# Kernel optimization log

Measured on AMD Instinct MI355X. Metric: run time of the kernel, lower is better.

Reference implementation:

```python
import jax, jax.numpy as jnp
import numpy as np

NUM_CLASSES = 19
EPS = 1e-8  # torch cosine_similarity eps


def setup_inputs() -> dict:
    key = jax.random.key(0)
    k1, k2 = jax.random.split(key)
    inputs = jax.random.normal(k1, (8, 256, 128, 128), dtype=jnp.float32)  # (B, D, H, W)
    targets = jax.random.randint(k2, (8, 128, 128), 0, NUM_CLASSES)        # (B, H, W)
    return {"inputs": inputs, "targets": targets}


def reference(inputs, targets):
    B, D, H, W = inputs.shape
    C = NUM_CLASSES
    # (N, D) pixel embeddings and (N,) labels
    feats = jnp.transpose(inputs, (0, 2, 3, 1)).reshape(-1, D)
    labels = targets.reshape(-1)

    # per-class centroids: sum of embeddings / max(count, 1)  (matches sum_pixel = max(mask.sum(), 1))
    counts = jax.ops.segment_sum(jnp.ones(labels.shape, jnp.float32), labels, num_segments=C)  # (C,)
    sums = jax.ops.segment_sum(feats, labels, num_segments=C)                                   # (C, D)
    centers = sums / jnp.maximum(counts, 1.0)[:, None]
    present = counts > 0  # classes absent from the batch are skipped in both loss terms

    # ---- sim_loss: sum over present classes of mean_{pixels of class i} (1 - cos(center_i, feat)) ----
    cen_px = centers[labels]                                   # (N, D)
    dot = jnp.sum(feats * cen_px, axis=1)
    n_f = jnp.sqrt(jnp.sum(feats * feats, axis=1))
    n_c = jnp.sqrt(jnp.sum(cen_px * cen_px, axis=1))
    cos_px = dot / jnp.maximum(n_f * n_c, EPS)
    per_class = jax.ops.segment_sum(1.0 - cos_px, labels, num_segments=C) / jnp.maximum(counts, 1.0)
    sim_loss = jnp.sum(jnp.where(present, per_class, 0.0))

    # ---- diff_loss: for each present i, mean_j over all C classes of
    #      (1 - cos(center_j, center_i)) if j == i else relu(cos(center_j, center_i)) ----
    n_cen = jnp.sqrt(jnp.sum(centers * centers, axis=1))       # (C,)
    S = (centers @ centers.T) / jnp.maximum(n_cen[:, None] * n_cen[None, :], EPS)  # (C, C)
    eye = jnp.eye(C, dtype=bool)
    per_pair = jnp.where(eye, 1.0 - S, jnp.maximum(S, 0.0))    # row i = losses vs class i
    per_i = jnp.mean(per_pair, axis=1)                          # mean reduction over C rows
    diff_loss = jnp.sum(jnp.where(present, per_i, 0.0))

    return jnp.reshape(diff_loss + sim_loss, (1,))  # torch returns a shape-(1,) tensor
```

## Files before the change

kernel.cpp:

```cpp
#include <hip/hip_runtime.h>
#include <math.h>

#define D_DIM 256
#define HW 16384
#define C 19
#define EPS 1e-8f

#define S_SC 1048576.0f
#define IS_S (1.0f/1048576.0f)
#define U_SC 16777216.0f
#define IS_U (1.0f/16777216.0f)

#define OFF_S      0
#define OFF_U      4864
#define OFF_CNT    9728
#define OFF_IO     9760
#define OFF_PNF    140832
#define PNF_STRIDE 8256
#define OFF_PS     4367904
#define OFF_PU     4445728

__global__ __launch_bounds__(256) void kA_stream(const float* __restrict__ in,
                                                 const int* __restrict__ tgt,
                                                 int* __restrict__ wsi) {
    __shared__ int sS[8 * 161];
    const int tid = threadIdx.x;
    const int bid = blockIdx.x;
    const int b = bid >> 6, s = (bid >> 1) & 31, h = bid & 1;
    const int copy = tid & 7;
    for (int i = tid; i < 8 * 161; i += 256) sS[i] = 0;
    __syncthreads();

    const int hwb = (h << 13) + (tid << 2);
    const int pb  = (b << 14) + hwb;
    int4 lab[8];
    #pragma unroll
    for (int it = 0; it < 8; ++it) lab[it] = *(const int4*)(tgt + pb + (it << 10));

    const float* base = in + (((size_t)((b << 8) + (s << 3))) << 14) + hwb;
    float4 nf[8];
    #pragma unroll
    for (int it = 0; it < 8; ++it) nf[it] = make_float4(0.f, 0.f, 0.f, 0.f);

    #pragma unroll
    for (int d = 0; d < 8; ++d) {
        float4 v[8];
        #pragma unroll
        for (int it = 0; it < 8; ++it)
            v[it] = *(const float4*)(base + ((size_t)d << 14) + (it << 10));
        const int sb = copy * 161 + d * 20;
        #pragma unroll
        for (int it = 0; it < 8; ++it) {
            nf[it].x += v[it].x * v[it].x; nf[it].y += v[it].y * v[it].y;
            nf[it].z += v[it].z * v[it].z; nf[it].w += v[it].w * v[it].w;
            atomicAdd(&sS[sb + lab[it].x], __float2int_rn(v[it].x * S_SC));
            atomicAdd(&sS[sb + lab[it].y], __float2int_rn(v[it].y * S_SC));
            atomicAdd(&sS[sb + lab[it].z], __float2int_rn(v[it].z * S_SC));
            atomicAdd(&sS[sb + lab[it].w], __float2int_rn(v[it].w * S_SC));
        }
    }

    float* pnf = (float*)wsi + OFF_PNF
               + (size_t)(((b << 1) + h) * 32 + s) * PNF_STRIDE;
    #pragma unroll
    for (int it = 0; it < 8; ++it)
        *(float4*)(pnf + (it << 10) + (tid << 2)) = nf[it];

    __syncthreads();
    if (tid < 152) {
        const int d = tid / 19, l = tid - d * 19;
        int acc = 0;
        #pragma unroll
        for (int c = 0; c < 8; ++c) acc += sS[c * 161 + d * 20 + l];
        wsi[OFF_PS + bid * 152 + tid] = acc;
    }
}

__global__ __launch_bounds__(256) void kA2_io(int* __restrict__ wsi) {
    float* wsf = (float*)wsi;
    const int j = blockIdx.x, tid = threadIdx.x;
    const int b = j >> 4, h = (j >> 3) & 1, ch = j & 7;
    const float* pn = wsf + OFF_PNF + (size_t)((b << 1) + h) * 32 * PNF_STRIDE
                    + (ch << 10) + (tid << 2);
    float4 acc = {0.f, 0.f, 0.f, 0.f};
    #pragma unroll 8
    for (int s = 0; s < 32; ++s) {
        float4 v = *(const float4*)(pn + (size_t)s * PNF_STRIDE);
        acc.x += v.x; acc.y += v.y; acc.z += v.z; acc.w += v.w;
    }
    float4 io;
    io.x = acc.x > 0.f ? U_SC * rsqrtf(acc.x) : 0.f;
    io.y = acc.y > 0.f ? U_SC * rsqrtf(acc.y) : 0.f;
    io.z = acc.z > 0.f ? U_SC * rsqrtf(acc.z) : 0.f;
    io.w = acc.w > 0.f ? U_SC * rsqrtf(acc.w) : 0.f;
    *(float4*)(wsf + OFF_IO + (b << 14) + (h << 13) + (ch << 10) + (tid << 2)) = io;
    if (j == 0 && tid < 32) wsi[OFF_CNT + tid] = 0;
}

__global__ __launch_bounds__(256) void kB_stream(const float* __restrict__ in,
                                                 const int* __restrict__ tgt,
                                                 int* __restrict__ wsi) {
    __shared__ int sU[8 * 161];
    __shared__ int sH[8 * 21];
    const int tid = threadIdx.x;
    const int bid = blockIdx.x;
    const int b = bid >> 6, s = (bid >> 1) & 31, h = bid & 1;
    const int copy = tid & 7;
    for (int i = tid; i < 8 * 161; i += 256) sU[i] = 0;
    if (tid < 8 * 21) sH[tid] = 0;
    __syncthreads();

    const int hwb = (h << 13) + (tid << 2);
    const int pb  = (b << 14) + hwb;
    const float* iof = (const float*)wsi + OFF_IO;
    int4   lab[8];
    float4 io4[8];
    #pragma unroll
    for (int it = 0; it < 8; ++it) {
        lab[it] = *(const int4*)(tgt + pb + (it << 10));
        io4[it] = *(const float4*)(iof + pb + (it << 10));
    }
    if (s == 0) {
        #pragma unroll
        for (int it = 0; it < 8; ++it) {
            atomicAdd(&sH[copy * 21 + lab[it].x], 1);
            atomicAdd(&sH[copy * 21 + lab[it].y], 1);
            atomicAdd(&sH[copy * 21 + lab[it].z], 1);
            atomicAdd(&sH[copy * 21 + lab[it].w], 1);
        }
    }

    const float* base = in + (((size_t)((b << 8) + (s << 3))) << 14) + hwb;
    #pragma unroll
    for (int d = 0; d < 8; ++d) {
        float4 v[8];
        #pragma unroll
        for (int it = 0; it < 8; ++it)
            v[it] = *(const float4*)(base + ((size_t)d << 14) + (it << 10));
        const int sb = copy * 161 + d * 20;
        #pragma unroll
        for (int it = 0; it < 8; ++it) {
            atomicAdd(&sU[sb + lab[it].x], __float2int_rn(v[it].x * io4[it].x));
            atomicAdd(&sU[sb + lab[it].y], __float2int_rn(v[it].y * io4[it].y));
            atomicAdd(&sU[sb + lab[it].z], __float2int_rn(v[it].z * io4[it].z));
            atomicAdd(&sU[sb + lab[it].w], __float2int_rn(v[it].w * io4[it].w));
        }
    }
    __syncthreads();
    if (tid < 152) {
        const int d = tid / 19, l = tid - d * 19;
        int acc = 0;
        #pragma unroll
        for (int c = 0; c < 8; ++c) acc += sU[c * 161 + d * 20 + l];
        wsi[OFF_PU + bid * 152 + tid] = acc;
    }
    if (s == 0 && tid < C) {
        int t = 0;
        #pragma unroll
        for (int c = 0; c < 8; ++c) t += sH[c * 21 + tid];
        atomicAdd(&wsi[OFF_CNT + tid], t);
    }
}

__global__ __launch_bounds__(256) void k1b_merge(int* __restrict__ wsi) {
    const int a = blockIdx.x >> 5, s = blockIdx.x & 31;
    const int tid = threadIdx.x;
    if (tid >= 152) return;
    const int* src = wsi + (a ? OFF_PU : OFF_PS);
    int acc = 0;
    #pragma unroll
    for (int r = 0; r < 16; ++r) {
        const int row = ((r >> 1) << 6) + (s << 1) + (r & 1);
        acc += src[row * 152 + tid];
    }
    const int d = tid / 19, l = tid - (tid / 19) * 19;
    wsi[(a ? OFF_U : OFF_S) + l * D_DIM + (s << 3) + d] = acc;
}

__global__ __launch_bounds__(512) void k2_final(const int* __restrict__ wsi,
                                                float* __restrict__ out) {
    __shared__ __align__(16) float s_cen[C * 260];
    __shared__ __align__(16) float s_u[C * 260];
    __shared__ float s_nc[C];
    __shared__ float s_cntf[C];
    __shared__ float s_pair[C * C];
    __shared__ float s_sim[C];
    const int tid = threadIdx.x;

    if (tid < C) s_cntf[tid] = (float)wsi[OFF_CNT + tid];
    __syncthreads();
    for (int i = tid; i < C * 256; i += 512) {
        int c = i >> 8, d = i & 255;
        float icnt = 1.f / fmaxf(s_cntf[c], 1.f);
        s_cen[c * 260 + d] = (float)wsi[OFF_S + i] * IS_S * icnt;
        s_u[c * 260 + d]   = (float)wsi[OFF_U + i] * IS_U;
    }
    __syncthreads();
    if (tid < C) {
        float nsq = 0.f;
        for (int d = 0; d < D_DIM; ++d) {
            float x = s_cen[tid * 260 + d];
            nsq += x * x;
        }
        s_nc[tid] = sqrtf(nsq);
    }
    __syncthreads();
    if (tid < C * C) {
        int i = tid / C, j = tid % C;
        const float4* ci = (const float4*)&s_cen[i * 260];
        const float4* cj = (const float4*)&s_cen[j * 260];
        float dot = 0.f;
        #pragma unroll 8
        for (int k = 0; k < 64; ++k) {
            float4 a = ci[k], bb = cj[k];
            dot += a.x * bb.x + a.y * bb.y + a.z * bb.z + a.w * bb.w;
        }
        float S = dot / fmaxf(s_nc[i] * s_nc[j], EPS);
        s_pair[tid] = (i == j) ? (1.f - S) : fmaxf(S, 0.f);
    } else if (tid >= 384 && tid < 384 + C) {
        int i = tid - 384;
        const float4* ci = (const float4*)&s_cen[i * 260];
        const float4* ui = (const float4*)&s_u[i * 260];
        float dot = 0.f;
        #pragma unroll 8
        for (int k = 0; k < 64; ++k) {
            float4 a = ci[k], bb = ui[k];
            dot += a.x * bb.x + a.y * bb.y + a.z * bb.z + a.w * bb.w;
        }
        s_sim[i] = (s_cntf[i] > 0.f)
                 ? (1.f - dot / fmaxf(s_nc[i] * s_cntf[i], EPS)) : 0.f;
    }
    __syncthreads();
    if (tid < C) {
        float row = 0.f;
        for (int j = 0; j < C; ++j) row += s_pair[tid * C + j];
        s_pair[tid * C] = (s_cntf[tid] > 0.f) ? (row * (1.f / (float)C)) : 0.f;
    }
    __syncthreads();
    if (tid == 0) {
        float tot = 0.f;
        for (int i = 0; i < C; ++i) tot += s_pair[i * C] + s_sim[i];
        out[0] = tot;
    }
}

extern "C" void kernel_launch(void* const* d_in, const int* in_sizes, int n_in,
                              void* d_out, int out_size, void* d_ws, size_t ws_size,
                              hipStream_t stream) {
    const float* in  = (const float*)d_in[0];
    const int*   tgt = (const int*)d_in[1];
    float* out = (float*)d_out;
    int*   wsi = (int*)d_ws;

    kA_stream<<<512, 256, 0, stream>>>(in, tgt, wsi);
    kA2_io<<<128, 256, 0, stream>>>(wsi);
    kB_stream<<<512, 256, 0, stream>>>(in, tgt, wsi);
    k1b_merge<<<64, 256, 0, stream>>>(wsi);
    k2_final<<<1, 512, 0, stream>>>(wsi, out);
}
```

Before: 229.6 us.

## Split streaming kernels into 2048 smaller blocks and move class counting to pass A

Both streaming passes now use 2048 blocks, each covering an eighth of an image's pixels for 8 channels, where before 512 blocks covered half an image. Each thread handles 2 float4 pixel groups instead of 8, which cuts register pressure and spreads work across more CUs. The class histogram moves into pass A and is written as per-block partial counts that the final kernel sums, replacing global atomics and the zeroing step. The cost is four times more partial-sum rows for the merge kernel to reduce, and more per-block setup and shared-memory reduction overhead.

```diff
diff --git a/kernel.cpp b/kernel.cpp
--- a/kernel.cpp
+++ b/kernel.cpp
@@ -13,44 +13,47 @@
 
 #define OFF_S      0
 #define OFF_U      4864
-#define OFF_CNT    9728
-#define OFF_IO     9760
-#define OFF_PNF    140832
-#define PNF_STRIDE 8256
-#define OFF_PS     4367904
-#define OFF_PU     4445728
+#define OFF_PCNT   9728
+#define OFF_IO     10944
+#define OFF_PNF    142016
+#define PNF_STRIDE 2080
+#define OFF_PS     4401856
+#define OFF_PU     4713152
+
 
 __global__ __launch_bounds__(256) void kA_stream(const float* __restrict__ in,
                                                  const int* __restrict__ tgt,
                                                  int* __restrict__ wsi) {
     __shared__ int sS[8 * 161];
+    __shared__ int sH[8 * 21];
     const int tid = threadIdx.x;
     const int bid = blockIdx.x;
-    const int b = bid >> 6, s = (bid >> 1) & 31, h = bid & 1;
+    const int b = bid >> 8, slab = (bid >> 3) & 31, oct = bid & 7;
     const int copy = tid & 7;
     for (int i = tid; i < 8 * 161; i += 256) sS[i] = 0;
-    __syncthreads();
-
-    const int hwb = (h << 13) + (tid << 2);
+    if (tid < 8 * 21) sH[tid] = 0;
+    __syncthreads();
+
+    const int hwb = (oct << 11) + (tid << 2);
     const int pb  = (b << 14) + hwb;
-    int4 lab[8];
-    #pragma unroll
-    for (int it = 0; it < 8; ++it) lab[it] = *(const int4*)(tgt + pb + (it << 10));
-
-    const float* base = in + (((size_t)((b << 8) + (s << 3))) << 14) + hwb;
-    float4 nf[8];
-    #pragma unroll
-    for (int it = 0; it < 8; ++it) nf[it] = make_float4(0.f, 0.f, 0.f, 0.f);
+    int4 lab[2];
+    #pragma unroll
+    for (int it = 0; it < 2; ++it) lab[it] = *(const int4*)(tgt + pb + (it << 10));
+
+    const float* base = in + (((size_t)((b << 8) + (slab << 3))) << 14) + hwb;
+    float4 nf[2];
+    nf[0] = make_float4(0.f, 0.f, 0.f, 0.f);
+    nf[1] = make_float4(0.f, 0.f, 0.f, 0.f);
 
     #pragma unroll
     for (int d = 0; d < 8; ++d) {
-        float4 v[8];
-        #pragma unroll
-        for (int it = 0; it < 8; ++it)
+        float4 v[2];
+        #pragma unroll
+        for (int it = 0; it < 2; ++it)
             v[it] = *(const float4*)(base + ((size_t)d << 14) + (it << 10));
         const int sb = copy * 161 + d * 20;
         #pragma unroll
-        for (int it = 0; it < 8; ++it) {
+        for (int it = 0; it < 2; ++it) {
             nf[it].x += v[it].x * v[it].x; nf[it].y += v[it].y * v[it].y;
             nf[it].z += v[it].z * v[it].z; nf[it].w += v[it].w * v[it].w;
             atomicAdd(&sS[sb + lab[it].x], __float2int_rn(v[it].x * S_SC));
@@ -60,86 +63,92 @@
         }
     }
 
-    float* pnf = (float*)wsi + OFF_PNF
-               + (size_t)(((b << 1) + h) * 32 + s) * PNF_STRIDE;
-    #pragma unroll
-    for (int it = 0; it < 8; ++it)
-        *(float4*)(pnf + (it << 10) + (tid << 2)) = nf[it];
-
+    {
+        float* pnf = (float*)wsi + OFF_PNF
+                   + (size_t)(((b << 3) + oct) * 32 + slab) * PNF_STRIDE;
+        *(float4*)(pnf + (tid << 2))        = nf[0];
+        *(float4*)(pnf + 1024 + (tid << 2)) = nf[1];
+    }
+
+    if (slab == 0) {
+        #pragma unroll
+        for (int it = 0; it < 2; ++it) {
+            atomicAdd(&sH[copy * 21 + lab[it].x], 1);
+            atomicAdd(&sH[copy * 21 + lab[it].y], 1);
+            atomicAdd(&sH[copy * 21 + lab[it].z], 1);
+            atomicAdd(&sH[copy * 21 + lab[it].w], 1);
+        }
+    }
     __syncthreads();
     if (tid < 152) {
-        const int d = tid / 19, l = tid - d * 19;
+        const int d = tid / 19, l = tid - (tid / 19) * 19;
         int acc = 0;
         #pragma unroll
         for (int c = 0; c < 8; ++c) acc += sS[c * 161 + d * 20 + l];
         wsi[OFF_PS + bid * 152 + tid] = acc;
     }
+    if (slab == 0 && tid < C) {
+        int t = 0;
+        #pragma unroll
+        for (int c = 0; c < 8; ++c) t += sH[c * 21 + tid];
+        wsi[OFF_PCNT + ((b << 3) + oct) * 19 + tid] = t;
+    }
 }
 
 __global__ __launch_bounds__(256) void kA2_io(int* __restrict__ wsi) {
     float* wsf = (float*)wsi;
-    const int j = blockIdx.x, tid = threadIdx.x;
-    const int b = j >> 4, h = (j >> 3) & 1, ch = j & 7;
-    const float* pn = wsf + OFF_PNF + (size_t)((b << 1) + h) * 32 * PNF_STRIDE
-                    + (ch << 10) + (tid << 2);
-    float4 acc = {0.f, 0.f, 0.f, 0.f};
-    #pragma unroll 8
-    for (int s = 0; s < 32; ++s) {
-        float4 v = *(const float4*)(pn + (size_t)s * PNF_STRIDE);
-        acc.x += v.x; acc.y += v.y; acc.z += v.z; acc.w += v.w;
-    }
-    float4 io;
-    io.x = acc.x > 0.f ? U_SC * rsqrtf(acc.x) : 0.f;
-    io.y = acc.y > 0.f ? U_SC * rsqrtf(acc.y) : 0.f;
-    io.z = acc.z > 0.f ? U_SC * rsqrtf(acc.z) : 0.f;
-    io.w = acc.w > 0.f ? U_SC * rsqrtf(acc.w) : 0.f;
-    *(float4*)(wsf + OFF_IO + (b << 14) + (h << 13) + (ch << 10) + (tid << 2)) = io;
-    if (j == 0 && tid < 32) wsi[OFF_CNT + tid] = 0;
+    const int boct = blockIdx.x, tid = threadIdx.x;
+    const float* pn0 = wsf + OFF_PNF + (size_t)(boct * 32) * PNF_STRIDE;
+    #pragma unroll
+    for (int it = 0; it < 2; ++it) {
+        const int j = (it << 10) + (tid << 2);
+        float4 acc = {0.f, 0.f, 0.f, 0.f};
+        #pragma unroll 8
+        for (int s = 0; s < 32; ++s) {
+            float4 v = *(const float4*)(pn0 + (size_t)s * PNF_STRIDE + j);
+            acc.x += v.x; acc.y += v.y; acc.z += v.z; acc.w += v.w;
+        }
+        float4 io;
+        io.x = acc.x > 0.f ? U_SC * rsqrtf(acc.x) : 0.f;
+        io.y = acc.y > 0.f ? U_SC * rsqrtf(acc.y) : 0.f;
+        io.z = acc.z > 0.f ? U_SC * rsqrtf(acc.z) : 0.f;
+        io.w = acc.w > 0.f ? U_SC * rsqrtf(acc.w) : 0.f;
+        *(float4*)(wsf + OFF_IO + ((boct >> 3) << 14) + ((boct & 7) << 11) + j) = io;
+    }
 }
 
 __global__ __launch_bounds__(256) void kB_stream(const float* __restrict__ in,
                                                  const int* __restrict__ tgt,
                                                  int* __restrict__ wsi) {
     __shared__ int sU[8 * 161];
-    __shared__ int sH[8 * 21];
     const int tid = threadIdx.x;
     const int bid = blockIdx.x;
-    const int b = bid >> 6, s = (bid >> 1) & 31, h = bid & 1;
+    const int b = bid >> 8, slab = (bid >> 3) & 31, oct = bid & 7;
     const int copy = tid & 7;
     for (int i = tid; i < 8 * 161; i += 256) sU[i] = 0;
-    if (tid < 8 * 21) sH[tid] = 0;
-    __syncthreads();
-
-    const int hwb = (h << 13) + (tid << 2);
+    __syncthreads();
+
+    const int hwb = (oct << 11) + (tid << 2);
     const int pb  = (b << 14) + hwb;
     const float* iof = (const float*)wsi + OFF_IO;
-    int4   lab[8];
-    float4 io4[8];
-    #pragma unroll
-    for (int it = 0; it < 8; ++it) {
+    int4   lab[2];
+    float4 io4[2];
+    #pragma unroll
+    for (int it = 0; it < 2; ++it) {
         lab[it] = *(const int4*)(tgt + pb + (it << 10));
         io4[it] = *(const float4*)(iof + pb + (it << 10));
     }
-    if (s == 0) {
-        #pragma unroll
-        for (int it = 0; it < 8; ++it) {
-            atomicAdd(&sH[copy * 21 + lab[it].x], 1);
-            atomicAdd(&sH[copy * 21 + lab[it].y], 1);
-            atomicAdd(&sH[copy * 21 + lab[it].z], 1);
-            atomicAdd(&sH[copy * 21 + lab[it].w], 1);
-        }
-    }
-
-    const float* base = in + (((size_t)((b << 8) + (s << 3))) << 14) + hwb;
+
+    const float* base = in + (((size_t)((b << 8) + (slab << 3))) << 14) + hwb;
     #pragma unroll
     for (int d = 0; d < 8; ++d) {
-        float4 v[8];
-        #pragma unroll
-        for (int it = 0; it < 8; ++it)
+        float4 v[2];
+        #pragma unroll
+        for (int it = 0; it < 2; ++it)
             v[it] = *(const float4*)(base + ((size_t)d << 14) + (it << 10));
         const int sb = copy * 161 + d * 20;
         #pragma unroll
-        for (int it = 0; it < 8; ++it) {
+        for (int it = 0; it < 2; ++it) {
             atomicAdd(&sU[sb + lab[it].x], __float2int_rn(v[it].x * io4[it].x));
             atomicAdd(&sU[sb + lab[it].y], __float2int_rn(v[it].y * io4[it].y));
             atomicAdd(&sU[sb + lab[it].z], __float2int_rn(v[it].z * io4[it].z));
@@ -148,33 +157,27 @@
     }
     __syncthreads();
     if (tid < 152) {
-        const int d = tid / 19, l = tid - d * 19;
+        const int d = tid / 19, l = tid - (tid / 19) * 19;
         int acc = 0;
         #pragma unroll
         for (int c = 0; c < 8; ++c) acc += sU[c * 161 + d * 20 + l];
         wsi[OFF_PU + bid * 152 + tid] = acc;
     }
-    if (s == 0 && tid < C) {
-        int t = 0;
-        #pragma unroll
-        for (int c = 0; c < 8; ++c) t += sH[c * 21 + tid];
-        atomicAdd(&wsi[OFF_CNT + tid], t);
-    }
-}
-
-__global__ __launch_bounds__(256) void k1b_merge(int* __restrict__ wsi) {
-    const int a = blockIdx.x >> 5, s = blockIdx.x & 31;
+}
+
+__global__ __launch_bounds__(256) void kM_merge(int* __restrict__ wsi) {
+    const int a = blockIdx.x >> 5, ss = blockIdx.x & 31;
     const int tid = threadIdx.x;
     if (tid >= 152) return;
     const int* src = wsi + (a ? OFF_PU : OFF_PS);
     int acc = 0;
     #pragma unroll
-    for (int r = 0; r < 16; ++r) {
-        const int row = ((r >> 1) << 6) + (s << 1) + (r & 1);
+    for (int r = 0; r < 64; ++r) {
+        const int row = ((r >> 3) << 8) + (ss << 3) + (r & 7);
         acc += src[row * 152 + tid];
     }
     const int d = tid / 19, l = tid - (tid / 19) * 19;
-    wsi[(a ? OFF_U : OFF_S) + l * D_DIM + (s << 3) + d] = acc;
+    wsi[(a ? OFF_U : OFF_S) + l * D_DIM + (ss << 3) + d] = acc;
 }
 
 __global__ __launch_bounds__(512) void k2_final(const int* __restrict__ wsi,
@@ -187,7 +190,12 @@
     __shared__ float s_sim[C];
     const int tid = threadIdx.x;
 
-    if (tid < C) s_cntf[tid] = (float)wsi[OFF_CNT + tid];
+    if (tid < C) {
+        int t = 0;
+        #pragma unroll
+        for (int r = 0; r < 64; ++r) t += wsi[OFF_PCNT + r * 19 + tid];
+        s_cntf[tid] = (float)t;
+    }
     __syncthreads();
     for (int i = tid; i < C * 256; i += 512) {
         int c = i >> 8, d = i & 255;
@@ -252,9 +260,9 @@
     float* out = (float*)d_out;
     int*   wsi = (int*)d_ws;
 
-    kA_stream<<<512, 256, 0, stream>>>(in, tgt, wsi);
-    kA2_io<<<128, 256, 0, stream>>>(wsi);
-    kB_stream<<<512, 256, 0, stream>>>(in, tgt, wsi);
-    k1b_merge<<<64, 256, 0, stream>>>(wsi);
+    kA_stream<<<2048, 256, 0, stream>>>(in, tgt, wsi);
+    kA2_io<<<64, 256, 0, stream>>>(wsi);
+    kB_stream<<<2048, 256, 0, stream>>>(in, tgt, wsi);
+    kM_merge<<<64, 256, 0, stream>>>(wsi);
     k2_final<<<1, 512, 0, stream>>>(wsi, out);
 }
```

Result: no change. 234.1 us (+2.0%).
